# Performance work log

Measured on AMD Instinct MI355X. Metric: run time of the kernel, lower is better.

The kernel has to match this reference:

```python
import jax, jax.numpy as jnp
import numpy as np

N_DIM = 768
HIDDEN_DIM = 768
BATCH = 4
SEQ = 2048


def setup_inputs() -> dict:
    key = jax.random.key(0)
    ks = jax.random.split(key, 9)
    s_in = 1.0 / np.sqrt(N_DIM)
    s_h = 1.0 / np.sqrt(HIDDEN_DIM)
    return {
        "x": jax.random.normal(ks[0], (BATCH, SEQ, N_DIM), dtype=jnp.float32),
        # torch Linear weights: [out_features, in_features]
        "wq": jax.random.uniform(ks[1], (HIDDEN_DIM, N_DIM), jnp.float32, -s_in, s_in),
        "bq": jax.random.uniform(ks[2], (HIDDEN_DIM,), jnp.float32, -s_in, s_in),
        "wk": jax.random.uniform(ks[3], (HIDDEN_DIM, N_DIM), jnp.float32, -s_in, s_in),
        "bk": jax.random.uniform(ks[4], (HIDDEN_DIM,), jnp.float32, -s_in, s_in),
        "wv": jax.random.uniform(ks[5], (HIDDEN_DIM, N_DIM), jnp.float32, -s_in, s_in),
        "bv": jax.random.uniform(ks[6], (HIDDEN_DIM,), jnp.float32, -s_in, s_in),
        "wo": jax.random.uniform(ks[7], (N_DIM, HIDDEN_DIM), jnp.float32, -s_h, s_h),
        "bo": jax.random.uniform(ks[8], (N_DIM,), jnp.float32, -s_h, s_h),
    }


def reference(x, wq, bq, wk, bk, wv, bv, wo, bo):
    # q,k,v: [B, S, H]
    q = jnp.einsum("bsd,hd->bsh", x, wq) + bq
    k = jnp.einsum("bsd,hd->bsh", x, wk) + bk
    v = jnp.einsum("bsd,hd->bsh", x, wv) + bv
    # NOTE: faithful to source — no 1/sqrt(d) scaling, no mask.
    scores = jnp.einsum("bqh,bkh->bqk", q, k)  # [B, S, S]
    attn = jax.nn.softmax(scores, axis=-1)
    y = jnp.einsum("bqk,bkh->bqh", attn, v)  # [B, S, H]
    out = jnp.einsum("bsh,dh->bsd", y, wo) + bo
    return out
```

## Files before the change

kernel.cpp:

```cpp
#include <hip/hip_runtime.h>

typedef _Float16 f16;
typedef _Float16 f16x8 __attribute__((ext_vector_type(8)));
typedef float f32x4 __attribute__((ext_vector_type(4)));

#define GLD16(g, l) __builtin_amdgcn_global_load_lds( \
    (const __attribute__((address_space(1))) void*)(g), \
    (__attribute__((address_space(3))) void*)(l), 16, 0, 0)

template <typename OutT, int BM, int BN, int MODE, int MINW>
__global__ __launch_bounds__(256, MINW)
void gemm_kernel(const f16* __restrict__ A, long sA,
                 const f16* __restrict__ B, long sB,
                 void* __restrict__ Cv, long sC,
                 void* __restrict__ C2v,
                 const float* __restrict__ bias,
                 const float* __restrict__ bias2,
                 int N, int K)
{
    constexpr int FM = BM / 32;
    constexpr int FN = BN / 32;
    constexpr int IA = BM / 32;
    constexpr int IB = BN / 32;

    OutT* C  = (OutT*)Cv;
    OutT* C2 = (OutT*)C2v;
    const int tid  = threadIdx.x;
    const int wave = tid >> 6;
    const int lane = tid & 63;
    const int bz   = blockIdx.z;
    A += (long)bz * sA;
    B += (long)bz * sB;
    C += (long)bz * sC;
    const long bm = (long)blockIdx.x * BM;
    const long bn = (long)blockIdx.y * BN;

    __shared__ f16 sAt[BM * 64];
    __shared__ f16 sBt[BN * 64];

    const int srow = lane >> 3;
    const int gch  = ((lane & 7) ^ srow) * 8;

    const f16* gAb = A + (bm + wave * (BM / 4) + srow) * (long)K + gch;
    const f16* gBb = B + (bn + wave * (BN / 4) + srow) * (long)K + gch;

    const int wm = (wave >> 1) * (BM / 2);
    const int wn = (wave & 1) * (BN / 2);
    const int lr = lane & 15;
    const int qd = lane >> 4;
    const int swz0 = ((0 * 4 + qd) ^ (lr & 7)) * 8;
    const int swz1 = ((1 * 4 + qd) ^ (lr & 7)) * 8;

    f32x4 acc[FM][FN] = {};

    for (int k0 = 0; k0 < K; k0 += 64) {
        #pragma unroll
        for (int i = 0; i < IA; ++i)
            GLD16(gAb + k0 + (long)i * 8 * K, &sAt[(wave * (BM / 4) + i * 8) * 64]);
        #pragma unroll
        for (int i = 0; i < IB; ++i)
            GLD16(gBb + k0 + (long)i * 8 * K, &sBt[(wave * (BN / 4) + i * 8) * 64]);
        __syncthreads();

        #pragma unroll
        for (int h = 0; h < 2; ++h) {
            const int swz = h ? swz1 : swz0;
            f16x8 af[FM], bf[FN];
            #pragma unroll
            for (int t = 0; t < FM; ++t)
                af[t] = *(const f16x8*)&sAt[(wm + t * 16 + lr) * 64 + swz];
            #pragma unroll
            for (int t = 0; t < FN; ++t)
                bf[t] = *(const f16x8*)&sBt[(wn + t * 16 + lr) * 64 + swz];
            #pragma unroll
            for (int tm = 0; tm < FM; ++tm)
                #pragma unroll
                for (int tn = 0; tn < FN; ++tn)
                    acc[tm][tn] = __builtin_amdgcn_mfma_f32_16x16x32_f16(
                        af[tm], bf[tn], acc[tm][tn], 0, 0, 0);
        }
        __syncthreads();
    }

    #pragma unroll
    for (int tn = 0; tn < FN; ++tn) {
        const long col = bn + wn + tn * 16 + lr;
        OutT* dst = C;
        long cc = col, stride = N;
        float bc = 0.f;
        if (MODE == 1) bc = bias[col];
        if (MODE == 3) {
            stride = 768;
            if (col >= 768) { dst = C2; cc = col - 768; bc = bias2[cc]; }
            else            { bc = bias[cc]; }
        }
        #pragma unroll
        for (int tm = 0; tm < FM; ++tm) {
            #pragma unroll
            for (int r = 0; r < 4; ++r) {
                const long row = bm + wm + tm * 16 + qd * 4 + r;
                float v = acc[tm][tn][r] + bc;
                if (MODE == 2) v += bias[row];
                dst[row * stride + cc] = (OutT)v;
            }
        }
    }
}

__global__ __launch_bounds__(256)
void softmax_kernel(f16* __restrict__ S)
{
    const long row = blockIdx.x;
    f16* p = S + row * 2048;
    const int tid  = threadIdx.x;
    const int wave = tid >> 6;
    const int lane = tid & 63;

    f16x8 x = *(const f16x8*)&p[tid * 8];
    float v[8];
    float m = -1e30f;
    #pragma unroll
    for (int j = 0; j < 8; ++j) { v[j] = (float)x[j]; m = fmaxf(m, v[j]); }
    #pragma unroll
    for (int off = 32; off > 0; off >>= 1) m = fmaxf(m, __shfl_down(m, off));

    __shared__ float rm[4], rs[4];
    if (lane == 0) rm[wave] = m;
    __syncthreads();
    m = fmaxf(fmaxf(rm[0], rm[1]), fmaxf(rm[2], rm[3]));

    float s = 0.f;
    #pragma unroll
    for (int j = 0; j < 8; ++j) { v[j] = __expf(v[j] - m); s += v[j]; }
    #pragma unroll
    for (int off = 32; off > 0; off >>= 1) s += __shfl_down(s, off);
    if (lane == 0) rs[wave] = s;
    __syncthreads();
    s = rs[0] + rs[1] + rs[2] + rs[3];
    const float inv = 1.0f / s;

    f16x8 y;
    #pragma unroll
    for (int j = 0; j < 8; ++j) y[j] = (f16)(v[j] * inv);
    *(f16x8*)&p[tid * 8] = y;
}

__global__ __launch_bounds__(256)
void cvt_all_kernel(const float* __restrict__ x,
                    const float* __restrict__ w0, const float* __restrict__ w1,
                    const float* __restrict__ w2, const float* __restrict__ w3,
                    f16* __restrict__ x16, f16* __restrict__ w16)
{
    const float* in; f16* out; long i;
    if (blockIdx.x < 3072) {
        in = x; out = x16;
        i = ((long)blockIdx.x * 256 + threadIdx.x) * 8;
    } else {
        const int wb  = blockIdx.x - 3072;
        const int sel = wb / 288;
        in  = (sel == 0) ? w0 : (sel == 1) ? w1 : (sel == 2) ? w2 : w3;
        out = w16 + (long)sel * 589824;
        i = ((long)(wb - sel * 288) * 256 + threadIdx.x) * 8;
    }
    float4 a = *(const float4*)(in + i);
    float4 b = *(const float4*)(in + i + 4);
    f16x8 o;
    o[0] = (f16)a.x; o[1] = (f16)a.y; o[2] = (f16)a.z; o[3] = (f16)a.w;
    o[4] = (f16)b.x; o[5] = (f16)b.y; o[6] = (f16)b.z; o[7] = (f16)b.w;
    *(f16x8*)&out[i] = o;
}

extern "C" void kernel_launch(void* const* d_in, const int* in_sizes, int n_in,
                              void* d_out, int out_size, void* d_ws, size_t ws_size,
                              hipStream_t stream)
{
    const float* x  = (const float*)d_in[0];
    const float* wq = (const float*)d_in[1];
    const float* bq = (const float*)d_in[2];
    const float* wk = (const float*)d_in[3];
    const float* bk = (const float*)d_in[4];
    const float* wv = (const float*)d_in[5];
    const float* bv = (const float*)d_in[6];
    const float* wo = (const float*)d_in[7];
    const float* bo = (const float*)d_in[8];

    char* ws = (char*)d_ws;
    f16* x16 = (f16*)(ws + 0);
    f16* w16 = (f16*)(ws + 12582912);
    f16* Q   = (f16*)(ws + 17301504);
    f16* Kb  = (f16*)(ws + 29884416);
    f16* VT  = (f16*)(ws + 42467328);
    f16* S   = (f16*)(ws + 55050240);
    f16* Y   = (f16*)(ws + 88604672);

    f16* wv16 = w16 + 2 * 589824;
    f16* wo16 = w16 + 3 * 589824;

    cvt_all_kernel<<<4224, 256, 0, stream>>>(x, wq, wk, wv, wo, x16, w16);

    gemm_kernel<f16, 128, 128, 3, 3><<<dim3(64, 12, 1), 256, 0, stream>>>(
        x16, 0, w16, 0, Q, 0, Kb, bq, bk, 1536, 768);
    gemm_kernel<f16, 64, 128, 2, 4><<<dim3(12, 16, 4), 256, 0, stream>>>(
        wv16, 0, x16, (long)2048 * 768, VT, (long)768 * 2048, nullptr,
        bv, nullptr, 2048, 768);
    gemm_kernel<f16, 128, 256, 0, 2><<<dim3(16, 8, 4), 256, 0, stream>>>(
        Q, (long)2048 * 768, Kb, (long)2048 * 768, S, (long)2048 * 2048,
        nullptr, nullptr, nullptr, 2048, 768);
    softmax_kernel<<<8192, 256, 0, stream>>>(S);
    gemm_kernel<f16, 128, 64, 0, 4><<<dim3(16, 12, 4), 256, 0, stream>>>(
        S, (long)2048 * 2048, VT, (long)768 * 2048, Y, (long)2048 * 768,
        nullptr, nullptr, nullptr, 768, 2048);
    gemm_kernel<float, 128, 64, 1, 4><<<dim3(64, 12, 1), 256, 0, stream>>>(
        Y, 0, wo16, 0, (float*)d_out, 0, nullptr, bo, nullptr, 768, 768);
}
```

Baseline: 224.6 us.

## Fuse Q/K/V projections into one GEMM with transposed V epilogue; retile PV and output GEMMs

The separate QK projection GEMM and the V-transpose GEMM are merged into a single 2304-wide GEMM over x16 and the concatenated weights. Its epilogue routes columns to Q, K or a transposed VT layout with the matching bias. This removes one launch and one extra read of x. The PV and output-projection GEMMs move from 128x64 to 128x128 tiles, which gives fewer blocks with more reuse per block. The VT writes from the fused epilogue are strided and uncoalesced, which may cost bandwidth.

```diff
diff --git a/kernel.cpp b/kernel.cpp
--- a/kernel.cpp
+++ b/kernel.cpp
@@ -13,9 +13,10 @@
 void gemm_kernel(const f16* __restrict__ A, long sA,
                  const f16* __restrict__ B, long sB,
                  void* __restrict__ Cv, long sC,
-                 void* __restrict__ C2v,
+                 void* __restrict__ C2v, void* __restrict__ C3v,
                  const float* __restrict__ bias,
                  const float* __restrict__ bias2,
+                 const float* __restrict__ bias3,
                  int N, int K)
 {
     constexpr int FM = BM / 32;
@@ -24,7 +25,6 @@
     constexpr int IB = BN / 32;
 
     OutT* C  = (OutT*)Cv;
-    OutT* C2 = (OutT*)C2v;
     const int tid  = threadIdx.x;
     const int wave = tid >> 6;
     const int lane = tid & 63;
@@ -85,23 +85,35 @@
     #pragma unroll
     for (int tn = 0; tn < FN; ++tn) {
         const long col = bn + wn + tn * 16 + lr;
-        OutT* dst = C;
-        long cc = col, stride = N;
-        float bc = 0.f;
-        if (MODE == 1) bc = bias[col];
-        if (MODE == 3) {
-            stride = 768;
-            if (col >= 768) { dst = C2; cc = col - 768; bc = bias2[cc]; }
-            else            { bc = bias[cc]; }
-        }
-        #pragma unroll
-        for (int tm = 0; tm < FM; ++tm) {
-            #pragma unroll
-            for (int r = 0; r < 4; ++r) {
-                const long row = bm + wm + tm * 16 + qd * 4 + r;
-                float v = acc[tm][tn][r] + bc;
-                if (MODE == 2) v += bias[row];
-                dst[row * stride + cc] = (OutT)v;
+        if (MODE == 4) {
+            const int  region = (int)(col >> 8) / 3;
+            const long cc = col - (long)region * 768;
+            const float bc = (region == 0) ? bias[cc]
+                           : (region == 1) ? bias2[cc] : bias3[cc];
+            #pragma unroll
+            for (int tm = 0; tm < FM; ++tm) {
+                #pragma unroll
+                for (int r = 0; r < 4; ++r) {
+                    const long row = bm + wm + tm * 16 + qd * 4 + r;
+                    const float v = acc[tm][tn][r] + bc;
+                    if (region == 0)
+                        ((f16*)Cv)[row * 768 + cc] = (f16)v;
+                    else if (region == 1)
+                        ((f16*)C2v)[row * 768 + cc] = (f16)v;
+                    else
+                        ((f16*)C3v)[(row >> 11) * (768L * 2048) + cc * 2048
+                                    + (row & 2047)] = (f16)v;
+                }
+            }
+        } else {
+            const float bc = (MODE == 1) ? bias[col] : 0.f;
+            #pragma unroll
+            for (int tm = 0; tm < FM; ++tm) {
+                #pragma unroll
+                for (int r = 0; r < 4; ++r) {
+                    const long row = bm + wm + tm * 16 + qd * 4 + r;
+                    C[row * (long)N + col] = (OutT)(acc[tm][tn][r] + bc);
+                }
             }
         }
     }
@@ -193,23 +205,20 @@
     f16* S   = (f16*)(ws + 55050240);
     f16* Y   = (f16*)(ws + 88604672);
 
-    f16* wv16 = w16 + 2 * 589824;
     f16* wo16 = w16 + 3 * 589824;
 
     cvt_all_kernel<<<4224, 256, 0, stream>>>(x, wq, wk, wv, wo, x16, w16);
 
-    gemm_kernel<f16, 128, 128, 3, 3><<<dim3(64, 12, 1), 256, 0, stream>>>(
-        x16, 0, w16, 0, Q, 0, Kb, bq, bk, 1536, 768);
-    gemm_kernel<f16, 64, 128, 2, 4><<<dim3(12, 16, 4), 256, 0, stream>>>(
-        wv16, 0, x16, (long)2048 * 768, VT, (long)768 * 2048, nullptr,
-        bv, nullptr, 2048, 768);
+    gemm_kernel<f16, 128, 256, 4, 2><<<dim3(64, 9, 1), 256, 0, stream>>>(
+        x16, 0, w16, 0, Q, 0, Kb, VT, bq, bk, bv, 2304, 768);
     gemm_kernel<f16, 128, 256, 0, 2><<<dim3(16, 8, 4), 256, 0, stream>>>(
         Q, (long)2048 * 768, Kb, (long)2048 * 768, S, (long)2048 * 2048,
-        nullptr, nullptr, nullptr, 2048, 768);
+        nullptr, nullptr, nullptr, nullptr, nullptr, 2048, 768);
     softmax_kernel<<<8192, 256, 0, stream>>>(S);
-    gemm_kernel<f16, 128, 64, 0, 4><<<dim3(16, 12, 4), 256, 0, stream>>>(
+    gemm_kernel<f16, 128, 128, 0, 3><<<dim3(16, 6, 4), 256, 0, stream>>>(
         S, (long)2048 * 2048, VT, (long)768 * 2048, Y, (long)2048 * 768,
-        nullptr, nullptr, nullptr, 768, 2048);
-    gemm_kernel<float, 128, 64, 1, 4><<<dim3(64, 12, 1), 256, 0, stream>>>(
-        Y, 0, wo16, 0, (float*)d_out, 0, nullptr, bo, nullptr, 768, 768);
-}
+        nullptr, nullptr, nullptr, nullptr, nullptr, 768, 2048);
+    gemm_kernel<float, 128, 128, 1, 3><<<dim3(64, 6, 1), 256, 0, stream>>>(
+        Y, 0, wo16, 0, (float*)d_out, 0, nullptr, nullptr, bo, nullptr,
+        nullptr, 768, 768);
+}
```

New measurement: 254.1 us. +13.1%, slower.
